# Kernel optimization log

Measured on AMD Instinct MI355X. Metric: run time of the kernel, lower is better.

The kernel has to match this reference:

```python
import jax, jax.numpy as jnp
import numpy as np
from jax.scipy.special import erf

B, S, D, H, F = 2, 2048, 1024, 16, 4096
EPS = 1e-5


def setup_inputs() -> dict:
    key = jax.random.key(0)
    ks = jax.random.split(key, 7)
    s = 0.02  # init scale so attention logits stay in a sane range
    return {
        "x": jax.random.normal(ks[0], (B, S, D), jnp.float32),
        "wq": jax.random.normal(ks[1], (D, D), jnp.float32) * s,
        "wk": jax.random.normal(ks[2], (D, D), jnp.float32) * s,
        "wv": jax.random.normal(ks[3], (D, D), jnp.float32) * s,
        "wo": jax.random.normal(ks[4], (D, D), jnp.float32) * s,
        "w1": jax.random.normal(ks[5], (F, D), jnp.float32) * s,
        "w2": jax.random.normal(ks[6], (D, F), jnp.float32) * s,
        "g1": jnp.ones((D,), jnp.float32),
        "g2": jnp.ones((D,), jnp.float32),
    }


def _rmsnorm(x, g):
    return x / jnp.sqrt(jnp.mean(x * x, axis=-1, keepdims=True) + EPS) * g


def _gelu_exact(x):
    # 0.5 * x * (1 + erf(x / sqrt(2)))
    return 0.5 * x * (1.0 + erf(x * (1.0 / np.sqrt(2.0).astype(np.float32))))


def reference(x, wq, wk, wv, wo, w1, w2, g1, g2):
    b, s, d = x.shape
    dk = d // H
    # --- attention sublayer (pre-RMSNorm) ---
    h = _rmsnorm(x, g1)
    # Linear(bias=False): y = h @ W.T; split heads -> [b, H, s, dk]
    q = (h @ wq.T).reshape(b, s, H, dk).transpose(0, 2, 1, 3)
    k = (h @ wk.T).reshape(b, s, H, dk).transpose(0, 2, 1, 3)
    v = (h @ wv.T).reshape(b, s, H, dk).transpose(0, 2, 1, 3)
    scores = jnp.einsum('bhqd,bhkd->bhqk', q, k) / jnp.sqrt(jnp.float32(dk))
    causal = jnp.triu(jnp.ones((s, s), bool), 1)  # True above diagonal -> masked
    scores = jnp.where(causal, -jnp.inf, scores)
    attn = jax.nn.softmax(scores, axis=-1)
    o = jnp.einsum('bhqk,bhkd->bhqd', attn, v)
    o = o.transpose(0, 2, 1, 3).reshape(b, s, d) @ wo.T
    x = x + o
    # --- FFN sublayer (pre-RMSNorm, exact-erf GELU) ---
    h2 = _rmsnorm(x, g2)
    f = _gelu_exact(h2 @ w1.T) @ w2.T
    return x + f
```

## Files before the change

kernel.cpp:

```cpp
#include <hip/hip_runtime.h>
#include <hip/hip_bf16.h>
#include <math.h>

#define B_   2
#define S_   2048
#define D_   1024
#define H_   16
#define DK_  64
#define F_   4096
#define NTOK (B_ * S_)

typedef __bf16 bf16x8 __attribute__((ext_vector_type(8)));
typedef float  f32x4  __attribute__((ext_vector_type(4)));

__device__ __forceinline__ unsigned short bf16r(float f) {
  unsigned u = __builtin_bit_cast(unsigned, f);
  u += 0x7fffu + ((u >> 16) & 1u);
  return (unsigned short)(u >> 16);
}

__device__ __forceinline__ void gload_lds16(const void* g, void* l) {
  __builtin_amdgcn_global_load_lds(
      (__attribute__((address_space(1))) void*)g,
      (__attribute__((address_space(3))) void*)l, 16, 0, 0);
}

__device__ __forceinline__ unsigned lds_off(void* p) {
  return (unsigned)(size_t)(__attribute__((address_space(3))) void*)p;
}
__device__ __forceinline__ bf16x8 ds_read16(unsigned a) {
  bf16x8 r;
  asm volatile("ds_read_b128 %0, %1" : "=v"(r) : "v"(a));
  return r;
}
__device__ __forceinline__ void ds_write32(unsigned a, unsigned v) {
  asm volatile("ds_write_b32 %0, %1" : : "v"(a), "v"(v));
}
__device__ __forceinline__ float fexp2(float x) {
  float r;
  asm volatile("v_exp_f32 %0, %1\n\ts_nop 0" : "=v"(r) : "v"(x));
  return r;
}

__device__ __forceinline__ float gelu_fast(float x) {
  float y = 0.7978845608f * x * (1.0f + 0.044715f * x * x);
  float e = fexp2(2.885390082f * y);
  float t = 1.0f - 2.0f / (e + 1.0f);
  return 0.5f * x * (1.0f + t);
}

struct CvtArgs {
  const float* src[6];
  unsigned short* dst[6];
  int start[7];
};
__global__ __launch_bounds__(256) void cvt_all_kernel(CvtArgs a) {
  int i = blockIdx.x * blockDim.x + threadIdx.x;
  if (i >= a.start[6]) return;
  int k = 0;
#pragma unroll
  for (int j = 1; j < 6; ++j)
    if (i >= a.start[j]) k = j;
  int off = i - a.start[k];
  float4 v = reinterpret_cast<const float4*>(a.src[k])[off];
  ushort4 o;
  o.x = bf16r(v.x); o.y = bf16r(v.y); o.z = bf16r(v.z); o.w = bf16r(v.w);
  reinterpret_cast<ushort4*>(a.dst[k])[off] = o;
}

__global__ __launch_bounds__(256) void rmsnorm_kernel(
    const float* __restrict__ x, const float* __restrict__ g,
    unsigned short* __restrict__ out) {
  int row = blockIdx.x;
  int t = threadIdx.x, lane = t & 63, w = t >> 6;
  float4 v = reinterpret_cast<const float4*>(x + (size_t)row * D_)[t];
  float ss = v.x * v.x + v.y * v.y + v.z * v.z + v.w * v.w;
#pragma unroll
  for (int d = 1; d < 64; d <<= 1) ss += __shfl_xor(ss, d);
  __shared__ float red[4];
  if (lane == 0) red[w] = ss;
  __syncthreads();
  float tot = red[0] + red[1] + red[2] + red[3];
  float rstd = rsqrtf(tot * (1.0f / D_) + 1e-5f);
  float4 gv = reinterpret_cast<const float4*>(g)[t];
  ushort4 o;
  o.x = bf16r(v.x * rstd * gv.x);
  o.y = bf16r(v.y * rstd * gv.y);
  o.z = bf16r(v.z * rstd * gv.z);
  o.w = bf16r(v.w * rstd * gv.w);
  reinterpret_cast<ushort4*>(out + (size_t)row * D_)[t] = o;
}

template <int EPI>
__device__ __forceinline__ void gemm128_body(
    const unsigned short* __restrict__ A, const unsigned short* __restrict__ Bw,
    int M, int N, int K,
    const float* __restrict__ resid, float* __restrict__ outF,
    unsigned short* __restrict__ outB, unsigned short* __restrict__ outB2,
    unsigned short* __restrict__ outB3) {
  constexpr int BUFU = 256 * 32;
  __shared__ __attribute__((aligned(16))) unsigned short lds[4 * BUFU];
  const int t = threadIdx.x, lane = t & 63, w = t >> 6;
  const int wm = w >> 2, wn = w & 3;
  const int lg = lane >> 4, ln = lane & 15;

  const int gx = gridDim.x;
  int bid = blockIdx.y * gx + blockIdx.x;
  int RX = gx >> 2, RY = gridDim.y >> 1;
  int xcd = bid & 7, c = bid >> 3;
  int bx = (xcd & 3) * RX + (c % RX);
  int by = (xcd >> 2) * RY + (c / RX);
  const int m0 = by * 128, n0 = bx * 128;

  const int nt = K >> 5;

  auto stage = [&](int tile) {
    const int buf = tile & 3;
    const int k0 = tile << 5;
    unsigned short* la = &lds[buf * BUFU];
    unsigned short* lb = la + 4096;
    int Ln = t >> 3, p = t & 7, u = p ^ (Ln & 7);
    int row = 2 * Ln + (u >> 2), cg = u & 3;
    gload_lds16(A + (size_t)(m0 + row) * K + k0 + cg * 8, &la[t * 8]);
    gload_lds16(Bw + (size_t)(n0 + row) * K + k0 + cg * 8, &lb[t * 8]);
  };

  stage(0);
  if (nt > 1) stage(1);
  if (nt > 2) stage(2);

  const unsigned base0 = lds_off(lds);
  unsigned offA[4], offB[2];
#pragma unroll
  for (int m = 0; m < 4; ++m) {
    int r = wm * 64 + m * 16 + ln;
    int Ln = r >> 1, p = ((r & 1) * 4 + lg) ^ (Ln & 7);
    offA[m] = (unsigned)((Ln * 64 + p * 8) * 2);
  }
#pragma unroll
  for (int n = 0; n < 2; ++n) {
    int r = wn * 32 + n * 16 + ln;
    int Ln = r >> 1, p = ((r & 1) * 4 + lg) ^ (Ln & 7);
    offB[n] = (unsigned)(8192 + (Ln * 64 + p * 8) * 2);
  }

  f32x4 acc[4][2] = {};

  for (int tile = 0; tile < nt; ++tile) {
    const int rem = nt - 1 - tile;
    if (rem >= 2)      { asm volatile("s_waitcnt vmcnt(4)"); }
    else if (rem == 1) { asm volatile("s_waitcnt vmcnt(2)"); }
    else               { asm volatile("s_waitcnt vmcnt(0)"); }
    __builtin_amdgcn_sched_barrier(0);
    __builtin_amdgcn_s_barrier();
    const unsigned bb = base0 + (unsigned)((tile & 3) * (BUFU * 2));
    bf16x8 af[4], bf[2];
#pragma unroll
    for (int m = 0; m < 4; ++m) af[m] = ds_read16(bb + offA[m]);
#pragma unroll
    for (int n = 0; n < 2; ++n) bf[n] = ds_read16(bb + offB[n]);
    if (tile + 3 < nt) stage(tile + 3);
    asm volatile("s_waitcnt lgkmcnt(0)");
    __builtin_amdgcn_sched_barrier(0);
    __builtin_amdgcn_s_setprio(1);
#pragma unroll
    for (int m = 0; m < 4; ++m)
#pragma unroll
      for (int n = 0; n < 2; ++n)
        acc[m][n] = __builtin_amdgcn_mfma_f32_16x16x32_bf16(af[m], bf[n], acc[m][n], 0, 0, 0);
    __builtin_amdgcn_s_setprio(0);
  }

  const int rbase = m0 + wm * 64 + lg * 4;
  const int cbase = n0 + wn * 32 + ln;
#pragma unroll
  for (int m = 0; m < 4; ++m) {
#pragma unroll
    for (int n = 0; n < 2; ++n) {
      int col = cbase + n * 16;
#pragma unroll
      for (int j = 0; j < 4; ++j) {
        int row = rbase + m * 16 + j;
        float v = acc[m][n][j];
        if (EPI == 1) {
          outB[(size_t)row * N + col] = bf16r(gelu_fast(v));
        } else if (EPI == 2) {
          outF[(size_t)row * N + col] = v + resid[(size_t)row * N + col];
        } else {
          if (col < D_) {
            outB[(size_t)row * D_ + col] = bf16r(v);
          } else if (col < 2 * D_) {
            outB2[(size_t)row * D_ + (col - D_)] = bf16r(v);
          } else {
            int bb2 = row >> 11, s = row & (S_ - 1);
            outB3[((size_t)(bb2 * D_) + (col - 2 * D_)) * S_ + s] = bf16r(v);
          }
        }
      }
    }
  }
}

__global__ __launch_bounds__(512, 4) void qkv_gemm(
    const unsigned short* __restrict__ A, const unsigned short* __restrict__ Bw,
    int M, int N, int K, unsigned short* o1, unsigned short* o2, unsigned short* o3) {
  gemm128_body<4>(A, Bw, M, N, K, nullptr, nullptr, o1, o2, o3);
}
__global__ __launch_bounds__(512, 4) void ffn1_gemm(
    const unsigned short* __restrict__ A, const unsigned short* __restrict__ Bw,
    int M, int N, int K, unsigned short* o1) {
  gemm128_body<1>(A, Bw, M, N, K, nullptr, nullptr, o1, nullptr, nullptr);
}
__global__ __launch_bounds__(512, 4) void wo_gemm(
    const unsigned short* __restrict__ A, const unsigned short* __restrict__ Bw,
    int M, int N, int K, const float* __restrict__ resid, float* __restrict__ outF) {
  gemm128_body<2>(A, Bw, M, N, K, resid, outF, nullptr, nullptr, nullptr);
}
__global__ __launch_bounds__(512, 4) void ffn2_gemm(
    const unsigned short* __restrict__ A, const unsigned short* __restrict__ Bw,
    int M, int N, int K, const float* __restrict__ resid, float* __restrict__ outF) {
  gemm128_body<2>(A, Bw, M, N, K, resid, outF, nullptr, nullptr, nullptr);
}

__global__ __launch_bounds__(512, 1) void attn_kernel(
    const unsigned short* __restrict__ qg, const unsigned short* __restrict__ kg,
    const unsigned short* __restrict__ vt, unsigned short* __restrict__ og) {
  __shared__ __attribute__((aligned(16))) unsigned short Kl[2][4096];
  __shared__ __attribute__((aligned(16))) unsigned short Vl[2][4096];
  __shared__ __attribute__((aligned(16))) unsigned short Pl[8][1024];
  const int t = threadIdx.x, lane = t & 63, w = t >> 6;
  const int lg = lane >> 4, ln = lane & 15;

  int bid = blockIdx.x;
  int nl = (bid & 7) * 64 + (bid >> 3);
  int bh = nl >> 4, qxr = nl & 15;
  int b = bh >> 4, h = bh & 15;
  int q0 = (15 - qxr) * 128;
  int qw = q0 + w * 16;

  bf16x8 aq[2];
  {
    const unsigned short* qp =
        qg + (size_t)(b * S_ + qw + ln) * D_ + h * DK_ + lg * 8;
    aq[0] = *reinterpret_cast<const bf16x8*>(qp);
    aq[1] = *reinterpret_cast<const bf16x8*>(qp + 32);
  }
  asm volatile("" : : "v"(aq[0]), "v"(aq[1]));

  float mr = -1e30f, lr = 0.f;
  f32x4 oacc[4] = {};
  const int dqt = qw >> 6;
  const int nt = (q0 >> 6) + 2;
  const float SCL = 0.125f * 1.44269504089f;

  auto stage = [&](int kt) {
    const int buf = kt & 1;
    const int kv0 = kt * 64;
    int row = t >> 3, cg = t & 7, sg = cg ^ (row & 7);
    gload_lds16(kg + (size_t)(b * S_ + kv0 + row) * D_ + h * DK_ + sg * 8, &Kl[buf][t * 8]);
    gload_lds16(vt + (size_t)(b * D_ + h * DK_ + row) * S_ + kv0 + sg * 8, &Vl[buf][t * 8]);
  };
  stage(0);

  const unsigned kbase = lds_off(&Kl[0][0]);
  const unsigned vbase = lds_off(&Vl[0][0]);
  const unsigned pbase = lds_off(&Pl[w][0]);

  for (int kt = 0; kt < nt; ++kt) {
    asm volatile("s_waitcnt vmcnt(0)");
    __builtin_amdgcn_sched_barrier(0);
    __builtin_amdgcn_s_barrier();
    const unsigned kb = kbase + (unsigned)((kt & 1) * 8192);
    const unsigned vb = vbase + (unsigned)((kt & 1) * 8192);
    const int kv0 = kt * 64;
    if (kt <= dqt) {
      f32x4 sc[4] = {};
      bf16x8 kf[4];
#pragma unroll
      for (int n = 0; n < 4; ++n) {
        int r = n * 16 + ln;
        int cg0 = lg ^ (r & 7);
        kf[n] = ds_read16(kb + (unsigned)((r * 64 + cg0 * 8) * 2));
      }
      if (kt + 1 < nt) stage(kt + 1);
      asm volatile("s_waitcnt lgkmcnt(0)");
      __builtin_amdgcn_sched_barrier(0);
#pragma unroll
      for (int n = 0; n < 4; ++n)
        sc[n] = __builtin_amdgcn_mfma_f32_16x16x32_bf16(kf[n], aq[0], sc[n], 0, 0, 0);
#pragma unroll
      for (int n = 0; n < 4; ++n) {
        int r = n * 16 + ln;
        int cg1 = (4 + lg) ^ (r & 7);
        kf[n] = ds_read16(kb + (unsigned)((r * 64 + cg1 * 8) * 2));
      }
      asm volatile("s_waitcnt lgkmcnt(0)");
      __builtin_amdgcn_sched_barrier(0);
#pragma unroll
      for (int n = 0; n < 4; ++n)
        sc[n] = __builtin_amdgcn_mfma_f32_16x16x32_bf16(kf[n], aq[1], sc[n], 0, 0, 0);
      const bool diag = (kt == dqt);
      const int qi = qw + ln;
      float mx = -1e30f;
#pragma unroll
      for (int n = 0; n < 4; ++n)
#pragma unroll
        for (int j = 0; j < 4; ++j) {
          float s = sc[n][j] * SCL;
          if (diag && (kv0 + n * 16 + lg * 4 + j) > qi) s = -1e30f;
          sc[n][j] = s;
          mx = fmaxf(mx, s);
        }
      mx = fmaxf(mx, __shfl_xor(mx, 16));
      mx = fmaxf(mx, __shfl_xor(mx, 32));
      float mn = fmaxf(mr, mx);
      float ps = 0.f;
#pragma unroll
      for (int n = 0; n < 4; ++n)
#pragma unroll
        for (int j = 0; j < 4; ++j) {
          float p = fexp2(sc[n][j] - mn);
          sc[n][j] = p;
          ps += p;
        }
      ps += __shfl_xor(ps, 16);
      ps += __shfl_xor(ps, 32);
      if (__all(mx <= mr)) {
        lr += ps;
      } else {
        float sf = fexp2(mr - mn);
        mr = mn;
        lr = lr * sf + ps;
#pragma unroll
        for (int j = 0; j < 4; ++j) {
          float sfj = __shfl(sf, lg * 4 + j);
#pragma unroll
          for (int f = 0; f < 4; ++f) oacc[f][j] *= sfj;
        }
      }
#pragma unroll
      for (int n = 0; n < 4; ++n) {
        int kvc = n * 16 + lg * 4;
        int cg = (kvc >> 3) ^ (ln & 7);
        unsigned pa_addr = pbase + (unsigned)((ln * 64 + cg * 8 + (kvc & 7)) * 2);
        unsigned p01 = (unsigned)bf16r(sc[n][0]) | ((unsigned)bf16r(sc[n][1]) << 16);
        unsigned p23 = (unsigned)bf16r(sc[n][2]) | ((unsigned)bf16r(sc[n][3]) << 16);
        ds_write32(pa_addr, p01);
        ds_write32(pa_addr + 4, p23);
      }
      asm volatile("s_waitcnt lgkmcnt(0)");
      __builtin_amdgcn_sched_barrier(0);
#pragma unroll
      for (int c = 0; c < 2; ++c) {
        unsigned cgp = (unsigned)((c * 4 + lg) ^ (ln & 7));
        bf16x8 pa = ds_read16(pbase + (unsigned)(ln * 128) + cgp * 16);
        bf16x8 vf[4];
#pragma unroll
        for (int f = 0; f < 4; ++f) {
          int dv = f * 16 + ln;
          int cgv = (c * 4 + lg) ^ (dv & 7);
          vf[f] = ds_read16(vb + (unsigned)((dv * 64 + cgv * 8) * 2));
        }
        asm volatile("s_waitcnt lgkmcnt(0)");
        __builtin_amdgcn_sched_barrier(0);
#pragma unroll
        for (int f = 0; f < 4; ++f)
          oacc[f] = __builtin_amdgcn_mfma_f32_16x16x32_bf16(pa, vf[f], oacc[f], 0, 0, 0);
      }
    }
  }
#pragma unroll
  for (int j = 0; j < 4; ++j) {
    float lj = __shfl(lr, lg * 4 + j);
    float inv = 1.0f / lj;
    int row = b * S_ + qw + lg * 4 + j;
#pragma unroll
    for (int f = 0; f < 4; ++f)
      og[(size_t)row * D_ + h * DK_ + f * 16 + ln] = bf16r(oacc[f][j] * inv);
  }
}

extern "C" void kernel_launch(void* const* d_in, const int* in_sizes, int n_in,
                              void* d_out, int out_size, void* d_ws, size_t ws_size,
                              hipStream_t stream) {
  const float* x  = (const float*)d_in[0];
  const float* wq = (const float*)d_in[1];
  const float* wk = (const float*)d_in[2];
  const float* wv = (const float*)d_in[3];
  const float* wo = (const float*)d_in[4];
  const float* w1 = (const float*)d_in[5];
  const float* w2 = (const float*)d_in[6];
  const float* g1 = (const float*)d_in[7];
  const float* g2 = (const float*)d_in[8];
  float* out = (float*)d_out;

  char* ws = (char*)d_ws;
  const size_t MB = 1024 * 1024;
  unsigned short* wqkv_b = (unsigned short*)(ws + 0 * MB);
  unsigned short* wo_b   = (unsigned short*)(ws + 6 * MB);
  unsigned short* w1_b   = (unsigned short*)(ws + 8 * MB);
  unsigned short* w2_b   = (unsigned short*)(ws + 16 * MB);
  unsigned short* h_b    = (unsigned short*)(ws + 24 * MB);
  unsigned short* q_b    = (unsigned short*)(ws + 32 * MB);
  unsigned short* k_b    = (unsigned short*)(ws + 40 * MB);
  unsigned short* vt_b   = (unsigned short*)(ws + 48 * MB);
  unsigned short* o_b    = (unsigned short*)(ws + 56 * MB);
  float*          x1     = (float*)(ws + 64 * MB);
  unsigned short* mid    = (unsigned short*)(ws + 80 * MB);

  CvtArgs ca;
  ca.src[0] = wq; ca.dst[0] = wqkv_b;
  ca.src[1] = wk; ca.dst[1] = wqkv_b + (size_t)D_ * D_;
  ca.src[2] = wv; ca.dst[2] = wqkv_b + (size_t)2 * D_ * D_;
  ca.src[3] = wo; ca.dst[3] = wo_b;
  ca.src[4] = w1; ca.dst[4] = w1_b;
  ca.src[5] = w2; ca.dst[5] = w2_b;
  int q4 = D_ * D_ / 4, f4 = F_ * D_ / 4;
  ca.start[0] = 0;
  ca.start[1] = q4;
  ca.start[2] = 2 * q4;
  ca.start[3] = 3 * q4;
  ca.start[4] = 4 * q4;
  ca.start[5] = 4 * q4 + f4;
  ca.start[6] = 4 * q4 + 2 * f4;
  cvt_all_kernel<<<(ca.start[6] + 255) / 256, 256, 0, stream>>>(ca);

  rmsnorm_kernel<<<NTOK, 256, 0, stream>>>(x, g1, h_b);

  qkv_gemm<<<dim3(3 * D_ / 128, NTOK / 128), dim3(512), 0, stream>>>(
      h_b, wqkv_b, NTOK, 3 * D_, D_, q_b, k_b, vt_b);

  attn_kernel<<<dim3(512), dim3(512), 0, stream>>>(q_b, k_b, vt_b, o_b);

  wo_gemm<<<dim3(D_ / 128, NTOK / 128), dim3(512), 0, stream>>>(
      o_b, wo_b, NTOK, D_, D_, x, x1);

  rmsnorm_kernel<<<NTOK, 256, 0, stream>>>(x1, g2, h_b);

  ffn1_gemm<<<dim3(F_ / 128, NTOK / 128), dim3(512), 0, stream>>>(
      h_b, w1_b, NTOK, F_, D_, mid);

  ffn2_gemm<<<dim3(D_ / 128, NTOK / 128), dim3(512), 0, stream>>>(
      mid, w2_b, NTOK, D_, F_, x1, out);
}
```

Baseline: 251.3 us.

## Use 256x128 tiles for QKV/FFN1 GEMMs and restructure causal attention kernel

Adds a 256x128 GEMM body with a triple-buffered LDS pipeline, used for the QKV and FFN1 projections, and folds the softmax scale and log2e into Q in the QKV epilogue. The attention kernel moves to 256-thread blocks with 64-row query tiles and 1024 blocks, applies the causal mask only on the last tile, defers the row-sum cross-lane reduction to the end, and packs P to bf16 with v_cvt_pk_bf16_f32. Together these aim to improve GEMM data reuse, raise attention occupancy, and cut per-tile ALU work. Larger tiles reduce the number of blocks and may leave GEMM grids less evenly spread across CUs, and pre-scaling Q in bf16 changes rounding slightly.

```diff
diff --git a/kernel.cpp b/kernel.cpp
--- a/kernel.cpp
+++ b/kernel.cpp
@@ -41,6 +41,11 @@
   asm volatile("v_exp_f32 %0, %1\n\ts_nop 0" : "=v"(r) : "v"(x));
   return r;
 }
+__device__ __forceinline__ unsigned cvt_pk_bf16(float lo, float hi) {
+  unsigned r;
+  asm volatile("v_cvt_pk_bf16_f32 %0, %1, %2" : "=v"(r) : "v"(lo), "v"(hi));
+  return r;
+}
 
 __device__ __forceinline__ float gelu_fast(float x) {
   float y = 0.7978845608f * x * (1.0f + 0.044715f * x * x);
@@ -48,6 +53,8 @@
   float t = 1.0f - 2.0f / (e + 1.0f);
   return 0.5f * x * (1.0f + t);
 }
+
+#define QSCL 0.18033688f
 
 struct CvtArgs {
   const float* src[6];
@@ -92,12 +99,143 @@
 }
 
 template <int EPI>
+__device__ __forceinline__ void gemm256_body(
+    const unsigned short* __restrict__ A, const unsigned short* __restrict__ Bw,
+    int M, int N, int K,
+    unsigned short* __restrict__ outB, unsigned short* __restrict__ outB2,
+    unsigned short* __restrict__ outB3) {
+  constexpr int BUFU = 12288;
+  __shared__ __attribute__((aligned(16))) unsigned short lds[3 * BUFU];
+  const int t = threadIdx.x, lane = t & 63, w = t >> 6;
+  const int wm = w >> 1, wn = w & 1;
+  const int lg = lane >> 4, ln = lane & 15;
+
+  const int gx = gridDim.x;
+  int bid = blockIdx.y * gx + blockIdx.x;
+  int xcd = bid & 7, c = bid >> 3;
+  int RX = gx >> 2, RY = gridDim.y >> 1;
+  int bx = (xcd & 3) * RX + (c % RX);
+  int by = (xcd >> 2) * RY + (c / RX);
+  const int m0 = by * 256, n0 = bx * 128;
+
+  const int nt = K >> 5;
+
+  auto stage = [&](int tile) {
+    int buf = tile % 3;
+    const int k0 = tile << 5;
+    unsigned short* la = &lds[buf * BUFU];
+    unsigned short* lb = la + 8192;
+#pragma unroll
+    for (int i = 0; i < 2; ++i) {
+      int g = i * 512 + t;
+      int Ln = g >> 3, p = g & 7, u = p ^ (Ln & 7);
+      int row = 2 * Ln + (u >> 2), cg = u & 3;
+      gload_lds16(A + (size_t)(m0 + row) * K + k0 + cg * 8, &la[g * 8]);
+    }
+    {
+      int Ln = t >> 3, p = t & 7, u = p ^ (Ln & 7);
+      int row = 2 * Ln + (u >> 2), cg = u & 3;
+      gload_lds16(Bw + (size_t)(n0 + row) * K + k0 + cg * 8, &lb[t * 8]);
+    }
+  };
+
+  stage(0);
+  stage(1);
+
+  const unsigned base0 = lds_off(lds);
+  unsigned offA[4], offB[4];
+#pragma unroll
+  for (int m = 0; m < 4; ++m) {
+    int r = wm * 64 + m * 16 + ln;
+    int Ln = r >> 1, p = ((r & 1) * 4 + lg) ^ (Ln & 7);
+    offA[m] = (unsigned)((Ln * 64 + p * 8) * 2);
+  }
+#pragma unroll
+  for (int n = 0; n < 4; ++n) {
+    int r = wn * 64 + n * 16 + ln;
+    int Ln = r >> 1, p = ((r & 1) * 4 + lg) ^ (Ln & 7);
+    offB[n] = (unsigned)(16384 + (Ln * 64 + p * 8) * 2);
+  }
+
+  f32x4 acc[4][4] = {};
+
+  for (int tile = 0; tile < nt; ++tile) {
+    if (tile + 1 < nt) { asm volatile("s_waitcnt vmcnt(3)"); }
+    else               { asm volatile("s_waitcnt vmcnt(0)"); }
+    __builtin_amdgcn_sched_barrier(0);
+    __builtin_amdgcn_s_barrier();
+    const unsigned bb = base0 + (unsigned)((tile % 3) * (BUFU * 2));
+    bf16x8 af[4], bf0, bf1;
+#pragma unroll
+    for (int m = 0; m < 4; ++m) af[m] = ds_read16(bb + offA[m]);
+    bf0 = ds_read16(bb + offB[0]);
+    bf1 = ds_read16(bb + offB[1]);
+    if (tile + 2 < nt) stage(tile + 2);
+    asm volatile("s_waitcnt lgkmcnt(0)");
+    __builtin_amdgcn_sched_barrier(0);
+    __builtin_amdgcn_s_setprio(1);
+#pragma unroll
+    for (int m = 0; m < 4; ++m) {
+      acc[m][0] = __builtin_amdgcn_mfma_f32_16x16x32_bf16(af[m], bf0, acc[m][0], 0, 0, 0);
+      acc[m][1] = __builtin_amdgcn_mfma_f32_16x16x32_bf16(af[m], bf1, acc[m][1], 0, 0, 0);
+    }
+    __builtin_amdgcn_s_setprio(0);
+    bf0 = ds_read16(bb + offB[2]);
+    bf1 = ds_read16(bb + offB[3]);
+    asm volatile("s_waitcnt lgkmcnt(0)");
+    __builtin_amdgcn_sched_barrier(0);
+    __builtin_amdgcn_s_setprio(1);
+#pragma unroll
+    for (int m = 0; m < 4; ++m) {
+      acc[m][2] = __builtin_amdgcn_mfma_f32_16x16x32_bf16(af[m], bf0, acc[m][2], 0, 0, 0);
+      acc[m][3] = __builtin_amdgcn_mfma_f32_16x16x32_bf16(af[m], bf1, acc[m][3], 0, 0, 0);
+    }
+    __builtin_amdgcn_s_setprio(0);
+  }
+
+  const int rbase = m0 + wm * 64 + lg * 4;
+  const int cbase = n0 + wn * 64 + ln;
+#pragma unroll
+  for (int m = 0; m < 4; ++m) {
+#pragma unroll
+    for (int n = 0; n < 4; ++n) {
+      int col = cbase + n * 16;
+#pragma unroll
+      for (int j = 0; j < 4; ++j) {
+        int row = rbase + m * 16 + j;
+        float v = acc[m][n][j];
+        if (EPI == 1) {
+          outB[(size_t)row * N + col] = bf16r(gelu_fast(v));
+        } else {
+          if (col < D_) {
+            outB[(size_t)row * D_ + col] = bf16r(v * QSCL);
+          } else if (col < 2 * D_) {
+            outB2[(size_t)row * D_ + (col - D_)] = bf16r(v);
+          } else {
+            int bb2 = row >> 11, s = row & (S_ - 1);
+            outB3[((size_t)(bb2 * D_) + (col - 2 * D_)) * S_ + s] = bf16r(v);
+          }
+        }
+      }
+    }
+  }
+}
+
+__global__ __launch_bounds__(512, 4) void qkv_gemm(
+    const unsigned short* __restrict__ A, const unsigned short* __restrict__ Bw,
+    int M, int N, int K, unsigned short* o1, unsigned short* o2, unsigned short* o3) {
+  gemm256_body<4>(A, Bw, M, N, K, o1, o2, o3);
+}
+__global__ __launch_bounds__(512, 4) void ffn1_gemm(
+    const unsigned short* __restrict__ A, const unsigned short* __restrict__ Bw,
+    int M, int N, int K, unsigned short* o1) {
+  gemm256_body<1>(A, Bw, M, N, K, o1, nullptr, nullptr);
+}
+
 __device__ __forceinline__ void gemm128_body(
     const unsigned short* __restrict__ A, const unsigned short* __restrict__ Bw,
     int M, int N, int K,
-    const float* __restrict__ resid, float* __restrict__ outF,
-    unsigned short* __restrict__ outB, unsigned short* __restrict__ outB2,
-    unsigned short* __restrict__ outB3) {
+    const float* __restrict__ resid, float* __restrict__ outF) {
   constexpr int BUFU = 256 * 32;
   __shared__ __attribute__((aligned(16))) unsigned short lds[4 * BUFU];
   const int t = threadIdx.x, lane = t & 63, w = t >> 6;
@@ -181,61 +319,37 @@
 #pragma unroll
       for (int j = 0; j < 4; ++j) {
         int row = rbase + m * 16 + j;
-        float v = acc[m][n][j];
-        if (EPI == 1) {
-          outB[(size_t)row * N + col] = bf16r(gelu_fast(v));
-        } else if (EPI == 2) {
-          outF[(size_t)row * N + col] = v + resid[(size_t)row * N + col];
-        } else {
-          if (col < D_) {
-            outB[(size_t)row * D_ + col] = bf16r(v);
-          } else if (col < 2 * D_) {
-            outB2[(size_t)row * D_ + (col - D_)] = bf16r(v);
-          } else {
-            int bb2 = row >> 11, s = row & (S_ - 1);
-            outB3[((size_t)(bb2 * D_) + (col - 2 * D_)) * S_ + s] = bf16r(v);
-          }
-        }
+        outF[(size_t)row * N + col] = acc[m][n][j] + resid[(size_t)row * N + col];
       }
     }
   }
 }
 
-__global__ __launch_bounds__(512, 4) void qkv_gemm(
-    const unsigned short* __restrict__ A, const unsigned short* __restrict__ Bw,
-    int M, int N, int K, unsigned short* o1, unsigned short* o2, unsigned short* o3) {
-  gemm128_body<4>(A, Bw, M, N, K, nullptr, nullptr, o1, o2, o3);
-}
-__global__ __launch_bounds__(512, 4) void ffn1_gemm(
-    const unsigned short* __restrict__ A, const unsigned short* __restrict__ Bw,
-    int M, int N, int K, unsigned short* o1) {
-  gemm128_body<1>(A, Bw, M, N, K, nullptr, nullptr, o1, nullptr, nullptr);
-}
 __global__ __launch_bounds__(512, 4) void wo_gemm(
     const unsigned short* __restrict__ A, const unsigned short* __restrict__ Bw,
     int M, int N, int K, const float* __restrict__ resid, float* __restrict__ outF) {
-  gemm128_body<2>(A, Bw, M, N, K, resid, outF, nullptr, nullptr, nullptr);
+  gemm128_body(A, Bw, M, N, K, resid, outF);
 }
 __global__ __launch_bounds__(512, 4) void ffn2_gemm(
     const unsigned short* __restrict__ A, const unsigned short* __restrict__ Bw,
     int M, int N, int K, const float* __restrict__ resid, float* __restrict__ outF) {
-  gemm128_body<2>(A, Bw, M, N, K, resid, outF, nullptr, nullptr, nullptr);
-}
-
-__global__ __launch_bounds__(512, 1) void attn_kernel(
+  gemm128_body(A, Bw, M, N, K, resid, outF);
+}
+
+__global__ __launch_bounds__(256, 4) void attn_kernel(
     const unsigned short* __restrict__ qg, const unsigned short* __restrict__ kg,
     const unsigned short* __restrict__ vt, unsigned short* __restrict__ og) {
   __shared__ __attribute__((aligned(16))) unsigned short Kl[2][4096];
   __shared__ __attribute__((aligned(16))) unsigned short Vl[2][4096];
-  __shared__ __attribute__((aligned(16))) unsigned short Pl[8][1024];
+  __shared__ __attribute__((aligned(16))) unsigned short Pl[4][1024];
   const int t = threadIdx.x, lane = t & 63, w = t >> 6;
   const int lg = lane >> 4, ln = lane & 15;
 
   int bid = blockIdx.x;
-  int nl = (bid & 7) * 64 + (bid >> 3);
-  int bh = nl >> 4, qxr = nl & 15;
+  int nl = (bid & 7) * 128 + (bid >> 3);
+  int bh = nl >> 5, qxr = nl & 31;
   int b = bh >> 4, h = bh & 15;
-  int q0 = (15 - qxr) * 128;
+  int q0 = (31 - qxr) * 64;
   int qw = q0 + w * 16;
 
   bf16x8 aq[2];
@@ -249,16 +363,18 @@
 
   float mr = -1e30f, lr = 0.f;
   f32x4 oacc[4] = {};
-  const int dqt = qw >> 6;
-  const int nt = (q0 >> 6) + 2;
-  const float SCL = 0.125f * 1.44269504089f;
+  const int nt = (q0 >> 6) + 1;
 
   auto stage = [&](int kt) {
     const int buf = kt & 1;
     const int kv0 = kt * 64;
-    int row = t >> 3, cg = t & 7, sg = cg ^ (row & 7);
-    gload_lds16(kg + (size_t)(b * S_ + kv0 + row) * D_ + h * DK_ + sg * 8, &Kl[buf][t * 8]);
-    gload_lds16(vt + (size_t)(b * D_ + h * DK_ + row) * S_ + kv0 + sg * 8, &Vl[buf][t * 8]);
+#pragma unroll
+    for (int i = 0; i < 2; ++i) {
+      int g = i * 256 + t;
+      int row = g >> 3, cg = g & 7, sg = cg ^ (row & 7);
+      gload_lds16(kg + (size_t)(b * S_ + kv0 + row) * D_ + h * DK_ + sg * 8, &Kl[buf][g * 8]);
+      gload_lds16(vt + (size_t)(b * D_ + h * DK_ + row) * S_ + kv0 + sg * 8, &Vl[buf][g * 8]);
+    }
   };
   stage(0);
 
@@ -266,109 +382,116 @@
   const unsigned vbase = lds_off(&Vl[0][0]);
   const unsigned pbase = lds_off(&Pl[w][0]);
 
-  for (int kt = 0; kt < nt; ++kt) {
-    asm volatile("s_waitcnt vmcnt(0)");
-    __builtin_amdgcn_sched_barrier(0);
-    __builtin_amdgcn_s_barrier();
+  auto ctile = [&](int kt, bool dm) {
     const unsigned kb = kbase + (unsigned)((kt & 1) * 8192);
     const unsigned vb = vbase + (unsigned)((kt & 1) * 8192);
-    const int kv0 = kt * 64;
-    if (kt <= dqt) {
-      f32x4 sc[4] = {};
-      bf16x8 kf[4];
-#pragma unroll
-      for (int n = 0; n < 4; ++n) {
-        int r = n * 16 + ln;
-        int cg0 = lg ^ (r & 7);
-        kf[n] = ds_read16(kb + (unsigned)((r * 64 + cg0 * 8) * 2));
+    f32x4 sc[4] = {};
+    bf16x8 kf[4];
+#pragma unroll
+    for (int n = 0; n < 4; ++n) {
+      int r = n * 16 + ln;
+      int cg0 = lg ^ (r & 7);
+      kf[n] = ds_read16(kb + (unsigned)((r * 64 + cg0 * 8) * 2));
+    }
+    if (!dm) stage(kt + 1);
+    asm volatile("s_waitcnt lgkmcnt(0)");
+    __builtin_amdgcn_sched_barrier(0);
+#pragma unroll
+    for (int n = 0; n < 4; ++n)
+      sc[n] = __builtin_amdgcn_mfma_f32_16x16x32_bf16(kf[n], aq[0], sc[n], 0, 0, 0);
+#pragma unroll
+    for (int n = 0; n < 4; ++n) {
+      int r = n * 16 + ln;
+      int cg1 = (4 + lg) ^ (r & 7);
+      kf[n] = ds_read16(kb + (unsigned)((r * 64 + cg1 * 8) * 2));
+    }
+    asm volatile("s_waitcnt lgkmcnt(0)");
+    __builtin_amdgcn_sched_barrier(0);
+#pragma unroll
+    for (int n = 0; n < 4; ++n)
+      sc[n] = __builtin_amdgcn_mfma_f32_16x16x32_bf16(kf[n], aq[1], sc[n], 0, 0, 0);
+    if (dm) {
+      const int kv0 = kt * 64;
+      const int qi = qw + ln;
+#pragma unroll
+      for (int n = 0; n < 4; ++n)
+#pragma unroll
+        for (int j = 0; j < 4; ++j)
+          if ((kv0 + n * 16 + lg * 4 + j) > qi) sc[n][j] = -1e30f;
+    }
+    float t0 = fmaxf(sc[0][0], sc[0][1]), t1 = fmaxf(sc[0][2], sc[0][3]);
+    float t2 = fmaxf(sc[1][0], sc[1][1]), t3 = fmaxf(sc[1][2], sc[1][3]);
+    float t4 = fmaxf(sc[2][0], sc[2][1]), t5 = fmaxf(sc[2][2], sc[2][3]);
+    float t6 = fmaxf(sc[3][0], sc[3][1]), t7 = fmaxf(sc[3][2], sc[3][3]);
+    t0 = fmaxf(t0, t1); t2 = fmaxf(t2, t3); t4 = fmaxf(t4, t5); t6 = fmaxf(t6, t7);
+    float mx = fmaxf(fmaxf(t0, t2), fmaxf(t4, t6));
+    mx = fmaxf(mx, __shfl_xor(mx, 16));
+    mx = fmaxf(mx, __shfl_xor(mx, 32));
+    float mn = fmaxf(mr, mx);
+    float ps = 0.f;
+#pragma unroll
+    for (int n = 0; n < 4; ++n)
+#pragma unroll
+      for (int j = 0; j < 4; ++j) {
+        float p = fexp2(sc[n][j] - mn);
+        sc[n][j] = p;
+        ps += p;
       }
-      if (kt + 1 < nt) stage(kt + 1);
-      asm volatile("s_waitcnt lgkmcnt(0)");
-      __builtin_amdgcn_sched_barrier(0);
-#pragma unroll
-      for (int n = 0; n < 4; ++n)
-        sc[n] = __builtin_amdgcn_mfma_f32_16x16x32_bf16(kf[n], aq[0], sc[n], 0, 0, 0);
-#pragma unroll
-      for (int n = 0; n < 4; ++n) {
-        int r = n * 16 + ln;
-        int cg1 = (4 + lg) ^ (r & 7);
-        kf[n] = ds_read16(kb + (unsigned)((r * 64 + cg1 * 8) * 2));
+    if (__all(mx <= mr)) {
+      lr += ps;
+    } else {
+      float sf = fexp2(mr - mn);
+      mr = mn;
+      lr = lr * sf + ps;
+#pragma unroll
+      for (int j = 0; j < 4; ++j) {
+        float sfj = __shfl(sf, lg * 4 + j);
+#pragma unroll
+        for (int f = 0; f < 4; ++f) oacc[f][j] *= sfj;
+      }
+    }
+#pragma unroll
+    for (int n = 0; n < 4; ++n) {
+      int kvc = n * 16 + lg * 4;
+      int cg = (kvc >> 3) ^ (ln & 7);
+      unsigned pa_addr = pbase + (unsigned)((ln * 64 + cg * 8 + (kvc & 7)) * 2);
+      ds_write32(pa_addr, cvt_pk_bf16(sc[n][0], sc[n][1]));
+      ds_write32(pa_addr + 4, cvt_pk_bf16(sc[n][2], sc[n][3]));
+    }
+    asm volatile("s_waitcnt lgkmcnt(0)");
+    __builtin_amdgcn_sched_barrier(0);
+#pragma unroll
+    for (int c = 0; c < 2; ++c) {
+      unsigned cgp = (unsigned)((c * 4 + lg) ^ (ln & 7));
+      bf16x8 pa = ds_read16(pbase + (unsigned)(ln * 128) + cgp * 16);
+      bf16x8 vf[4];
+#pragma unroll
+      for (int f = 0; f < 4; ++f) {
+        int dv = f * 16 + ln;
+        int cgv = (c * 4 + lg) ^ (dv & 7);
+        vf[f] = ds_read16(vb + (unsigned)((dv * 64 + cgv * 8) * 2));
       }
       asm volatile("s_waitcnt lgkmcnt(0)");
       __builtin_amdgcn_sched_barrier(0);
 #pragma unroll
-      for (int n = 0; n < 4; ++n)
-        sc[n] = __builtin_amdgcn_mfma_f32_16x16x32_bf16(kf[n], aq[1], sc[n], 0, 0, 0);
-      const bool diag = (kt == dqt);
-      const int qi = qw + ln;
-      float mx = -1e30f;
-#pragma unroll
-      for (int n = 0; n < 4; ++n)
-#pragma unroll
-        for (int j = 0; j < 4; ++j) {
-          float s = sc[n][j] * SCL;
-          if (diag && (kv0 + n * 16 + lg * 4 + j) > qi) s = -1e30f;
-          sc[n][j] = s;
-          mx = fmaxf(mx, s);
-        }
-      mx = fmaxf(mx, __shfl_xor(mx, 16));
-      mx = fmaxf(mx, __shfl_xor(mx, 32));
-      float mn = fmaxf(mr, mx);
-      float ps = 0.f;
-#pragma unroll
-      for (int n = 0; n < 4; ++n)
-#pragma unroll
-        for (int j = 0; j < 4; ++j) {
-          float p = fexp2(sc[n][j] - mn);
-          sc[n][j] = p;
-          ps += p;
-        }
-      ps += __shfl_xor(ps, 16);
-      ps += __shfl_xor(ps, 32);
-      if (__all(mx <= mr)) {
-        lr += ps;
-      } else {
-        float sf = fexp2(mr - mn);
-        mr = mn;
-        lr = lr * sf + ps;
-#pragma unroll
-        for (int j = 0; j < 4; ++j) {
-          float sfj = __shfl(sf, lg * 4 + j);
-#pragma unroll
-          for (int f = 0; f < 4; ++f) oacc[f][j] *= sfj;
-        }
-      }
-#pragma unroll
-      for (int n = 0; n < 4; ++n) {
-        int kvc = n * 16 + lg * 4;
-        int cg = (kvc >> 3) ^ (ln & 7);
-        unsigned pa_addr = pbase + (unsigned)((ln * 64 + cg * 8 + (kvc & 7)) * 2);
-        unsigned p01 = (unsigned)bf16r(sc[n][0]) | ((unsigned)bf16r(sc[n][1]) << 16);
-        unsigned p23 = (unsigned)bf16r(sc[n][2]) | ((unsigned)bf16r(sc[n][3]) << 16);
-        ds_write32(pa_addr, p01);
-        ds_write32(pa_addr + 4, p23);
-      }
-      asm volatile("s_waitcnt lgkmcnt(0)");
-      __builtin_amdgcn_sched_barrier(0);
-#pragma unroll
-      for (int c = 0; c < 2; ++c) {
-        unsigned cgp = (unsigned)((c * 4 + lg) ^ (ln & 7));
-        bf16x8 pa = ds_read16(pbase + (unsigned)(ln * 128) + cgp * 16);
-        bf16x8 vf[4];
-#pragma unroll
-        for (int f = 0; f < 4; ++f) {
-          int dv = f * 16 + ln;
-          int cgv = (c * 4 + lg) ^ (dv & 7);
-          vf[f] = ds_read16(vb + (unsigned)((dv * 64 + cgv * 8) * 2));
-        }
-        asm volatile("s_waitcnt lgkmcnt(0)");
-        __builtin_amdgcn_sched_barrier(0);
-#pragma unroll
-        for (int f = 0; f < 4; ++f)
-          oacc[f] = __builtin_amdgcn_mfma_f32_16x16x32_bf16(pa, vf[f], oacc[f], 0, 0, 0);
-      }
-    }
-  }
+      for (int f = 0; f < 4; ++f)
+        oacc[f] = __builtin_amdgcn_mfma_f32_16x16x32_bf16(pa, vf[f], oacc[f], 0, 0, 0);
+    }
+  };
+
+  for (int kt = 0; kt < nt - 1; ++kt) {
+    asm volatile("s_waitcnt vmcnt(0)");
+    __builtin_amdgcn_sched_barrier(0);
+    __builtin_amdgcn_s_barrier();
+    ctile(kt, false);
+  }
+  asm volatile("s_waitcnt vmcnt(0)");
+  __builtin_amdgcn_sched_barrier(0);
+  __builtin_amdgcn_s_barrier();
+  ctile(nt - 1, true);
+
+  lr += __shfl_xor(lr, 16);
+  lr += __shfl_xor(lr, 32);
 #pragma unroll
   for (int j = 0; j < 4; ++j) {
     float lj = __shfl(lr, lg * 4 + j);
@@ -427,17 +550,17 @@
 
   rmsnorm_kernel<<<NTOK, 256, 0, stream>>>(x, g1, h_b);
 
-  qkv_gemm<<<dim3(3 * D_ / 128, NTOK / 128), dim3(512), 0, stream>>>(
+  qkv_gemm<<<dim3(3 * D_ / 128, NTOK / 256), dim3(512), 0, stream>>>(
       h_b, wqkv_b, NTOK, 3 * D_, D_, q_b, k_b, vt_b);
 
-  attn_kernel<<<dim3(512), dim3(512), 0, stream>>>(q_b, k_b, vt_b, o_b);
+  attn_kernel<<<dim3(1024), dim3(256), 0, stream>>>(q_b, k_b, vt_b, o_b);
 
   wo_gemm<<<dim3(D_ / 128, NTOK / 128), dim3(512), 0, stream>>>(
       o_b, wo_b, NTOK, D_, D_, x, x1);
 
   rmsnorm_kernel<<<NTOK, 256, 0, stream>>>(x1, g2, h_b);
 
-  ffn1_gemm<<<dim3(F_ / 128, NTOK / 128), dim3(512), 0, stream>>>(
+  ffn1_gemm<<<dim3(F_ / 128, NTOK / 256), dim3(512), 0, stream>>>(
       h_b, w1_b, NTOK, F_, D_, mid);
 
   ffn2_gemm<<<dim3(D_ / 128, NTOK / 128), dim3(512), 0, stream>>>(
```

After: 248.8 us. No clear change (-1.0%).
